# Performance work log

Measured on AMD Instinct MI355X. Metric: run time of the kernel, lower is better.

Reference implementation:

```python
import jax, jax.numpy as jnp
import numpy as np

NEG_SLOPE = 0.2

def _gat_layer(x, src, dst, W, a_src, a_dst, b, n_nodes):
    # x: [N, Fin], W: [Fin, Fout], a_src/a_dst: [Fout], b: [Fout]
    h = x @ W                                  # [N, Fout]
    alpha_s = h @ a_src                        # [N]
    alpha_d = h @ a_dst                        # [N]
    e = jax.nn.leaky_relu(alpha_s[src] + alpha_d[dst], NEG_SLOPE)  # [E]
    # softmax over edges grouped by destination node
    m = jax.ops.segment_max(e, dst, num_segments=n_nodes)
    ex = jnp.exp(e - m[dst])
    denom = jax.ops.segment_sum(ex, dst, num_segments=n_nodes)
    alpha = ex / denom[dst]                    # [E]
    out = jax.ops.segment_sum(h[src] * alpha[:, None], dst, num_segments=n_nodes)
    return out + b


def setup_inputs() -> dict:
    key = jax.random.key(0)
    N, E, INP = 50000, 1600000, 128
    topo = [32, 64, 128, 128]
    OUT = 16
    ks = jax.random.split(key, 32)
    inp = {}
    inp['x'] = jax.random.normal(ks[0], (N, INP), dtype=jnp.float32)
    inp['edge_index'] = jax.random.randint(ks[1], (2, E), 0, N, dtype=jnp.int64)
    dims = [INP] + topo
    ki = 2
    for i in range(4):
        fin, fout = dims[i], dims[i + 1]
        s = 1.0 / np.sqrt(fin)
        inp[f'W{i}'] = jax.random.normal(ks[ki], (fin, fout), dtype=jnp.float32) * s; ki += 1
        inp[f'a_src{i}'] = jax.random.normal(ks[ki], (fout,), dtype=jnp.float32) * (1.0 / np.sqrt(fout)); ki += 1
        inp[f'a_dst{i}'] = jax.random.normal(ks[ki], (fout,), dtype=jnp.float32) * (1.0 / np.sqrt(fout)); ki += 1
        inp[f'b{i}'] = jnp.zeros((fout,), dtype=jnp.float32); ki += 1
    inp['fc_W'] = jax.random.normal(ks[ki], (topo[-1], OUT), dtype=jnp.float32) * (1.0 / np.sqrt(topo[-1])); ki += 1
    inp['fc_b'] = jnp.zeros((OUT,), dtype=jnp.float32)
    return inp


def reference(x, edge_index, W0, a_src0, a_dst0, b0, W1, a_src1, a_dst1, b1,
              W2, a_src2, a_dst2, b2, W3, a_src3, a_dst3, b3, fc_W, fc_b):
    n = x.shape[0]
    loops = jnp.arange(n, dtype=edge_index.dtype)
    src = jnp.concatenate([edge_index[0], loops])  # add self-loops (GATConv default)
    dst = jnp.concatenate([edge_index[1], loops])
    layers = [(W0, a_src0, a_dst0, b0), (W1, a_src1, a_dst1, b1),
              (W2, a_src2, a_dst2, b2), (W3, a_src3, a_dst3, b3)]
    for (W, a_s, a_d, b) in layers:
        x = jax.nn.relu(_gat_layer(x, src, dst, W, a_s, a_d, b, n))
    return x @ fc_W + fc_b
```

## Files before the change

### kernel.cpp

```cpp
#include <hip/hip_runtime.h>
#include <hip/hip_bf16.h>
#include <hip/hip_fp16.h>


__device__ __forceinline__ float bf2f(unsigned short w) {
    return __uint_as_float(((unsigned int)w) << 16);
}
__device__ __forceinline__ unsigned enc_f(float f) {
    unsigned u = __float_as_uint(f);
    return (u & 0x80000000u) ? ~u : (u | 0x80000000u);
}
__device__ __forceinline__ float dec_f(unsigned u) {
    unsigned v = (u & 0x80000000u) ? (u & 0x7FFFFFFFu) : ~u;
    return __uint_as_float(v);
}

#define ELL_K 96

__global__ void detect_kernel(const unsigned short* __restrict__ xw,
                              const int* __restrict__ ew,
                              int* __restrict__ flags,
                              unsigned* __restrict__ maxbuf)
{
    __shared__ int cnt_sane[256];
    __shared__ int cnt_nz[256];
    const int t = threadIdx.x;
    unsigned short w = xw[2 * t];
    int e = (w >> 7) & 0xff;
    cnt_sane[t] = (e >= 110 && e <= 133) ? 1 : 0;
    cnt_nz[t] = (ew[2 * t + 1] != 0) ? 1 : 0;
    if (t < 8) maxbuf[t] = 0u;
    __syncthreads();
    if (t == 0) {
        int s = 0, nz = 0;
        for (int i = 0; i < 256; ++i) { s += cnt_sane[i]; nz += cnt_nz[i]; }
        flags[0] = (s >= 128) ? 1 : 0;
        flags[1] = (nz == 0) ? 1 : 0;
    }
}

struct ParamPtrs {
    const void* src[18];
    int n[18];
    int off[18];
};

__global__ void convert_params_kernel(ParamPtrs pp, const int* __restrict__ flags,
                                      float* __restrict__ out)
{
    const int b = blockIdx.x;
    const int n = pp.n[b];
    const float* fp = (const float*)pp.src[b];
    const unsigned short* hp = (const unsigned short*)pp.src[b];
    const int bf = flags[0];
    float* o = out + pp.off[b];
    for (int i = threadIdx.x; i < n; i += blockDim.x)
        o[i] = bf ? bf2f(hp[i]) : fp[i];
}

__global__ void extract_count_kernel(const int* __restrict__ e, const int* __restrict__ flags,
                                     unsigned* __restrict__ sd, unsigned short* __restrict__ rank,
                                     int* __restrict__ deg, long long E, long long Et)
{
    long long t = (long long)blockIdx.x * blockDim.x + threadIdx.x;
    if (t >= Et) return;
    int s, d;
    if (t >= E) { s = (int)(t - E); d = s; }
    else if (flags[1]) { s = e[2 * t]; d = e[2 * E + 2 * t]; }
    else               { s = e[t];     d = e[E + t]; }
    sd[t] = (unsigned)s | ((unsigned)d << 16);
    rank[t] = (unsigned short)atomicAdd(&deg[d], 1);
}

__global__ __launch_bounds__(256) void ell_fill_bucket_kernel(
    const unsigned* __restrict__ sd, const unsigned short* __restrict__ rank,
    unsigned short* __restrict__ ell16, long long Et, int chunkSize, int shift)
{
    const int bucket = blockIdx.x & 7;
    const long long c0 = (long long)(blockIdx.x >> 3) * chunkSize;
    const long long c1 = min(c0 + (long long)chunkSize, Et);
    for (long long i = c0 + threadIdx.x; i < c1; i += 256) {
        const unsigned v = sd[i];
        const int d = (int)(v >> 16);
        const int r = (int)rank[i];
        if ((d >> shift) == bucket && r < ELL_K)
            ell16[(long long)d * ELL_K + r] = (unsigned short)(v & 0xffffu);
    }
}

struct Half4 { __half2 a, b; };

__device__ __forceinline__ void store4(float* h, long long idx, const float* a) {
    *(float4*)(h + idx) = make_float4(a[0], a[1], a[2], a[3]);
}
__device__ __forceinline__ void store4(__half* h, long long idx, const float* a) {
    Half4 v;
    v.a = __floats2half2_rn(a[0], a[1]);
    v.b = __floats2half2_rn(a[2], a[3]);
    *(Half4*)(h + idx) = v;
}

template <int FIN, int FOUT, typename OT>
__global__ __launch_bounds__(256) void gemm_alpha_kernel(
    const void* __restrict__ xv, const int* __restrict__ flags, int x_ext,
    const float* __restrict__ W, const float* __restrict__ a_src,
    const float* __restrict__ a_dst, const float* __restrict__ bias,
    OT* __restrict__ h,
    float* __restrict__ alpha_s, float* __restrict__ alpha_d,
    unsigned* __restrict__ maxSD, int has_alpha,
    int N, int relu_in, int has_bias)
{
    constexpr int CG = FOUT / 4;
    constexpr int RT = 256 / CG;
    constexpr int RR = 64 / RT;
    constexpr int TM = 64;
    constexpr int XP = FIN + 4;
    constexpr int Q  = FIN / 8;

    __shared__ float xs[TM * XP];
    __shared__ float red[2][TM][CG + 1];

    const int tx = threadIdx.x;
    const int cg = tx & (CG - 1);
    const int rt = tx / CG;
    const long long base = (long long)blockIdx.x * TM;

    const int xbf = x_ext ? flags[0] : 0;

    for (int idx = tx; idx < TM * Q; idx += 256) {
        const int r  = idx / Q;
        const int c8 = idx - r * Q;
        const long long grow = base + r;
        float v[8] = {0.f, 0.f, 0.f, 0.f, 0.f, 0.f, 0.f, 0.f};
        if (grow < N) {
            const long long gi = grow * FIN + 8 * c8;
            if (x_ext) {
                if (xbf) {
                    const unsigned short* xp = (const unsigned short*)xv + gi;
                    #pragma unroll
                    for (int u = 0; u < 8; ++u) v[u] = bf2f(xp[u]);
                } else {
                    const float4 f0 = *((const float4*)((const float*)xv + gi));
                    const float4 f1 = *((const float4*)((const float*)xv + gi + 4));
                    v[0] = f0.x; v[1] = f0.y; v[2] = f0.z; v[3] = f0.w;
                    v[4] = f1.x; v[5] = f1.y; v[6] = f1.z; v[7] = f1.w;
                }
            } else {
                const float4 raw = *((const float4*)((const __half*)xv + gi));
                const __half2* q = (const __half2*)&raw;
                const float2 a0 = __half22float2(q[0]);
                const float2 a1 = __half22float2(q[1]);
                const float2 a2 = __half22float2(q[2]);
                const float2 a3 = __half22float2(q[3]);
                v[0] = a0.x; v[1] = a0.y; v[2] = a1.x; v[3] = a1.y;
                v[4] = a2.x; v[5] = a2.y; v[6] = a3.x; v[7] = a3.y;
            }
            if (relu_in) {
                #pragma unroll
                for (int u = 0; u < 8; ++u) v[u] = fmaxf(v[u], 0.f);
            }
        }
        *(float4*)&xs[r * XP + 8 * c8]     = make_float4(v[0], v[1], v[2], v[3]);
        *(float4*)&xs[r * XP + 8 * c8 + 4] = make_float4(v[4], v[5], v[6], v[7]);
    }
    __syncthreads();

    float acc[RR][4];
    #pragma unroll
    for (int rr = 0; rr < RR; ++rr)
        { acc[rr][0] = acc[rr][1] = acc[rr][2] = acc[rr][3] = 0.f; }

    const int r0 = rt * RR;
    #pragma unroll 4
    for (int k = 0; k < FIN; ++k) {
        const float4 w4 = *(const float4*)(W + k * FOUT + 4 * cg);
        #pragma unroll
        for (int rr = 0; rr < RR; ++rr) {
            const float xval = xs[(r0 + rr) * XP + k];
            acc[rr][0] += xval * w4.x;
            acc[rr][1] += xval * w4.y;
            acc[rr][2] += xval * w4.z;
            acc[rr][3] += xval * w4.w;
        }
    }

    if (has_bias) {
        const float4 b4 = *(const float4*)(bias + 4 * cg);
        #pragma unroll
        for (int rr = 0; rr < RR; ++rr) {
            acc[rr][0] += b4.x; acc[rr][1] += b4.y;
            acc[rr][2] += b4.z; acc[rr][3] += b4.w;
        }
    }

    #pragma unroll
    for (int rr = 0; rr < RR; ++rr) {
        const long long grow = base + r0 + rr;
        if (grow < N)
            store4(h, grow * FOUT + 4 * cg, acc[rr]);
    }

    if (has_alpha) {
        const float4 as4 = *(const float4*)(a_src + 4 * cg);
        const float4 ad4 = *(const float4*)(a_dst + 4 * cg);
        #pragma unroll
        for (int rr = 0; rr < RR; ++rr) {
            red[0][r0 + rr][cg] = acc[rr][0] * as4.x + acc[rr][1] * as4.y
                                + acc[rr][2] * as4.z + acc[rr][3] * as4.w;
            red[1][r0 + rr][cg] = acc[rr][0] * ad4.x + acc[rr][1] * ad4.y
                                + acc[rr][2] * ad4.z + acc[rr][3] * ad4.w;
        }
        __syncthreads();
        if (tx < TM) {
            float ss = 0.f, sd = 0.f;
            #pragma unroll
            for (int j = 0; j < CG; ++j) {
                ss += red[0][tx][j];
                sd += red[1][tx][j];
            }
            const long long grow = base + tx;
            const bool valid = grow < N;
            if (valid) { alpha_s[grow] = ss; alpha_d[grow] = sd; }
            float ms = valid ? ss : -INFINITY;
            float md = valid ? sd : -INFINITY;
            #pragma unroll
            for (int off = 32; off > 0; off >>= 1) {
                ms = fmaxf(ms, __shfl_down(ms, off, 64));
                md = fmaxf(md, __shfl_down(md, off, 64));
            }
            if (tx == 0) {
                atomicMax(&maxSD[0], enc_f(ms));
                atomicMax(&maxSD[1], enc_f(md));
            }
        }
    }
}

template <int FOUT>
__global__ __launch_bounds__(256) void gat_gather_kernel(
    const int* __restrict__ deg, const unsigned short* __restrict__ ell16,
    const float* __restrict__ as, const float* __restrict__ ad,
    const unsigned* __restrict__ maxSD,
    const __half* __restrict__ h, const float* __restrict__ bias,
    __half* __restrict__ out, int N)
{
    constexpr int LPE = FOUT / 8;
    constexpr int EPJ = 64 / LPE;

    const int wslot = threadIdx.x >> 6;
    const int lane = threadIdx.x & 63;
    const int d = blockIdx.x * 4 + wslot;
    if (d >= N) return;

    const float M = dec_f(maxSD[0]) + dec_f(maxSD[1]);
    const int cnt_all = min(deg[d], ELL_K);
    const long long e0 = (long long)d * ELL_K;
    const float add = ad[d];

    const int sub = lane / LPE;
    const int fl  = (lane % LPE) * 8;

    float den = 0.f;
    float a0 = 0.f, a1 = 0.f, a2 = 0.f, a3 = 0.f;
    float a4 = 0.f, a5 = 0.f, a6 = 0.f, a7 = 0.f;
    for (int base = 0; base < cnt_all; base += 64) {
        const int e = base + lane;
        float p = 0.f;
        int s = 0;
        if (e < cnt_all) {
            s = (int)ell16[e0 + e];
            float v = as[s] + add;
            v = (v > 0.f) ? v : 0.2f * v;
            p = expf(v - M);
        }
        den += p;
        const int cnt = min(64, cnt_all - base);
        for (int j = 0; j < cnt; j += 4 * EPJ) {
            float pj[4];
            float4 hv[4];
            #pragma unroll
            for (int u = 0; u < 4; ++u) {
                const int jj = j + u * EPJ + sub;
                pj[u] = __shfl(p, jj, 64);
                const int sj = __shfl(s, jj, 64);
                hv[u] = *(const float4*)(h + (long long)sj * FOUT + fl);
            }
            #pragma unroll
            for (int u = 0; u < 4; ++u) {
                const __half2* q = (const __half2*)&hv[u];
                const float2 f0 = __half22float2(q[0]);
                const float2 f1 = __half22float2(q[1]);
                const float2 f2 = __half22float2(q[2]);
                const float2 f3 = __half22float2(q[3]);
                a0 += pj[u] * f0.x;  a1 += pj[u] * f0.y;
                a2 += pj[u] * f1.x;  a3 += pj[u] * f1.y;
                a4 += pj[u] * f2.x;  a5 += pj[u] * f2.y;
                a6 += pj[u] * f3.x;  a7 += pj[u] * f3.y;
            }
        }
    }
    #pragma unroll
    for (int off = 32; off > 0; off >>= 1)
        den += __shfl_down(den, off, 64);
    den = __shfl(den, 0, 64);
    const float inv = 1.f / den;

    #pragma unroll
    for (int off = 32; off >= LPE; off >>= 1) {
        a0 += __shfl_down(a0, off, 64);
        a1 += __shfl_down(a1, off, 64);
        a2 += __shfl_down(a2, off, 64);
        a3 += __shfl_down(a3, off, 64);
        a4 += __shfl_down(a4, off, 64);
        a5 += __shfl_down(a5, off, 64);
        a6 += __shfl_down(a6, off, 64);
        a7 += __shfl_down(a7, off, 64);
    }
    if (lane < LPE) {
        const float4 bA = *(const float4*)(bias + fl);
        const float4 bB = *(const float4*)(bias + fl + 4);
        float4 pack;
        __half2* q = (__half2*)&pack;
        q[0] = __floats2half2_rn(bA.x + a0 * inv, bA.y + a1 * inv);
        q[1] = __floats2half2_rn(bA.z + a2 * inv, bA.w + a3 * inv);
        q[2] = __floats2half2_rn(bB.x + a4 * inv, bB.y + a5 * inv);
        q[3] = __floats2half2_rn(bB.z + a6 * inv, bB.w + a7 * inv);
        *(float4*)(out + (long long)d * FOUT + fl) = pack;
    }
}

extern "C" void kernel_launch(void* const* d_in, const int* in_sizes, int n_in,
                              void* d_out, int out_size, void* d_ws, size_t ws_size,
                              hipStream_t stream)
{
    const int INP = 128;
    const int N = in_sizes[0] / INP;
    const long long E = in_sizes[1] / 2;
    const long long Et = E + N;

    const int Fin[4]  = {128, 32, 64, 128};
    const int Fout[4] = {32, 64, 128, 128};

    char* p = (char*)d_ws;
    auto alloc = [&](size_t bytes) {
        char* r = p;
        p += (bytes + 255) & ~(size_t)255;
        return r;
    };
    __half*   bufH    = (__half*)  alloc((size_t)N * 128 * sizeof(__half));
    __half*   bufX    = (__half*)  alloc((size_t)N * 128 * sizeof(__half));
    float*    as      = (float*)   alloc((size_t)N * sizeof(float));
    float*    ad      = (float*)   alloc((size_t)N * sizeof(float));
    int*      deg     = (int*)     alloc((size_t)N * sizeof(int));
    unsigned short* ell16 = (unsigned short*)alloc((size_t)N * ELL_K * sizeof(unsigned short));
    unsigned* maxbuf  = (unsigned*)alloc(64);
    int*      flags   = (int*)     alloc(64);
    float*    params  = (float*)   alloc(64 * 1024 * sizeof(float));
    (void)ws_size;

    unsigned* sdA = (unsigned*)bufX;
    unsigned short* rankA = (unsigned short*)(sdA + Et);

    detect_kernel<<<1, 256, 0, stream>>>((const unsigned short*)d_in[0],
                                         (const int*)d_in[1], flags, maxbuf);

    ParamPtrs pp;
    int off = 0;
    {
        int k = 0;
        for (int i = 0; i < 4; ++i) {
            pp.n[k++] = Fin[i] * Fout[i];
            pp.n[k++] = Fout[i];
            pp.n[k++] = Fout[i];
            pp.n[k++] = Fout[i];
        }
        pp.n[16] = 128 * 16;
        pp.n[17] = 16;
        for (int i = 0; i < 18; ++i) {
            pp.src[i] = d_in[2 + i];
            pp.off[i] = off;
            off += pp.n[i];
        }
    }
    convert_params_kernel<<<18, 256, 0, stream>>>(pp, flags, params);

    const float* Wl[4], *asr[4], *adt[4], *bl[4];
    for (int i = 0; i < 4; ++i) {
        Wl[i]  = params + pp.off[4 * i + 0];
        asr[i] = params + pp.off[4 * i + 1];
        adt[i] = params + pp.off[4 * i + 2];
        bl[i]  = params + pp.off[4 * i + 3];
    }
    const float* fcW = params + pp.off[16];
    const float* fcb = params + pp.off[17];

    const int* e32 = (const int*)d_in[1];

    {
        hipMemsetAsync(deg, 0, (size_t)N * sizeof(int), stream);
        int eblocks = (int)((Et + 255) / 256);
        extract_count_kernel<<<eblocks, 256, 0, stream>>>(e32, flags, sdA, rankA,
                                                          deg, E, Et);
        int shift = 0;
        while ((N >> shift) > 8) shift++;
        const int chunkSize = 4096;
        const int nchunks = (int)((Et + chunkSize - 1) / chunkSize);
        ell_fill_bucket_kernel<<<nchunks * 8, 256, 0, stream>>>(
            sdA, rankA, ell16, Et, chunkSize, shift);
    }

    const int gblocks = (N + 3) / 4;
    const int mblocks = (N + 63) / 64;
    const void* xin = d_in[0];

    gemm_alpha_kernel<128, 32, __half><<<mblocks, 256, 0, stream>>>(
        xin, flags, 1, Wl[0], asr[0], adt[0], nullptr, bufH, as, ad,
        maxbuf + 0, 1, N, 0, 0);
    gat_gather_kernel<32><<<gblocks, 256, 0, stream>>>(
        deg, ell16, as, ad, maxbuf + 0, bufH, bl[0], bufX, N);

    gemm_alpha_kernel<32, 64, __half><<<mblocks, 256, 0, stream>>>(
        bufX, flags, 0, Wl[1], asr[1], adt[1], nullptr, bufH, as, ad,
        maxbuf + 2, 1, N, 1, 0);
    gat_gather_kernel<64><<<gblocks, 256, 0, stream>>>(
        deg, ell16, as, ad, maxbuf + 2, bufH, bl[1], bufX, N);

    gemm_alpha_kernel<64, 128, __half><<<mblocks, 256, 0, stream>>>(
        bufX, flags, 0, Wl[2], asr[2], adt[2], nullptr, bufH, as, ad,
        maxbuf + 4, 1, N, 1, 0);
    gat_gather_kernel<128><<<gblocks, 256, 0, stream>>>(
        deg, ell16, as, ad, maxbuf + 4, bufH, bl[2], bufX, N);

    gemm_alpha_kernel<128, 128, __half><<<mblocks, 256, 0, stream>>>(
        bufX, flags, 0, Wl[3], asr[3], adt[3], nullptr, bufH, as, ad,
        maxbuf + 6, 1, N, 1, 0);
    gat_gather_kernel<128><<<gblocks, 256, 0, stream>>>(
        deg, ell16, as, ad, maxbuf + 6, bufH, bl[3], bufX, N);

    gemm_alpha_kernel<128, 16, float><<<mblocks, 256, 0, stream>>>(
        bufX, flags, 0, fcW, nullptr, nullptr, fcb,
        (float*)d_out, nullptr, nullptr, nullptr, 0, N, 1, 1);
}
```

Before: 538.2 us.

## Build ELL adjacency via per-chunk shared-memory histograms instead of global atomics

Replaces the per-edge global atomicAdd degree counting with per-chunk shared-memory histograms holding packed 8-bit counters, a column scan that produces per-chunk base offsets and degrees, and an ELL fill that assigns slots with shared-memory atomics. This removes heavily contended global atomics and the 16-bit rank array. It adds a histogram buffer of NCHUNK×N bytes, which costs extra memory traffic. The 8-bit packed counters could overflow when a chunk holds many edges to one node, though slots are clamped at ELL_K. Slot ordering within a node may differ from before.

```diff
diff --git a/kernel.cpp b/kernel.cpp
--- a/kernel.cpp
+++ b/kernel.cpp
@@ -16,6 +16,7 @@
 }
 
 #define ELL_K 96
+#define NCHUNK 256
 
 __global__ void detect_kernel(const unsigned short* __restrict__ xw,
                               const int* __restrict__ ew,
@@ -58,33 +59,122 @@
         o[i] = bf ? bf2f(hp[i]) : fp[i];
 }
 
-__global__ void extract_count_kernel(const int* __restrict__ e, const int* __restrict__ flags,
-                                     unsigned* __restrict__ sd, unsigned short* __restrict__ rank,
-                                     int* __restrict__ deg, long long E, long long Et)
-{
-    long long t = (long long)blockIdx.x * blockDim.x + threadIdx.x;
-    if (t >= Et) return;
-    int s, d;
-    if (t >= E) { s = (int)(t - E); d = s; }
-    else if (flags[1]) { s = e[2 * t]; d = e[2 * E + 2 * t]; }
-    else               { s = e[t];     d = e[E + t]; }
-    sd[t] = (unsigned)s | ((unsigned)d << 16);
-    rank[t] = (unsigned short)atomicAdd(&deg[d], 1);
-}
-
-__global__ __launch_bounds__(256) void ell_fill_bucket_kernel(
-    const unsigned* __restrict__ sd, const unsigned short* __restrict__ rank,
-    unsigned short* __restrict__ ell16, long long Et, int chunkSize, int shift)
-{
+__global__ __launch_bounds__(1024) void hist_pack_kernel(
+    const int* __restrict__ e, const int* __restrict__ flags,
+    unsigned* __restrict__ sd, unsigned* __restrict__ hist,
+    long long E, long long Et, int chunk, int NQ)
+{
+    extern __shared__ unsigned hcnt[];
+    const int c = blockIdx.x;
+    for (int i = threadIdx.x; i < NQ; i += 1024) hcnt[i] = 0u;
+    __syncthreads();
+    const int f64 = flags[1];
+    const long long c0 = (long long)c * chunk;
+    long long c1 = c0 + chunk; if (c1 > Et) c1 = Et;
+    for (long long t = c0 + threadIdx.x; t < c1; t += 1024) {
+        int s, d;
+        if (t >= E) { s = (int)(t - E); d = s; }
+        else if (f64) { s = e[2 * t]; d = e[2 * E + 2 * t]; }
+        else          { s = e[t];     d = e[E + t]; }
+        sd[t] = (unsigned)s | ((unsigned)d << 16);
+        atomicAdd(&hcnt[d >> 2], 1u << ((d & 3) << 3));
+    }
+    __syncthreads();
+    unsigned* hrow = hist + (size_t)c * NQ;
+    for (int i = threadIdx.x; i < NQ; i += 1024) hrow[i] = hcnt[i];
+}
+
+__global__ __launch_bounds__(256) void chunk_scan_kernel(
+    const unsigned* __restrict__ hist, unsigned* __restrict__ base32,
+    int* __restrict__ deg, int NQ, int N)
+{
+    __shared__ unsigned short sums[32][8][4];
+    const int dql = threadIdx.x & 31;
+    const int oct = threadIdx.x >> 5;
+    const int dq  = blockIdx.x * 32 + dql;
+    const int cbeg = oct * 32;
+
+    unsigned s0 = 0, s1 = 0, s2 = 0, s3 = 0;
+    if (dq < NQ) {
+        const unsigned* hp = hist + (size_t)cbeg * NQ + dq;
+        #pragma unroll 8
+        for (int c = 0; c < 32; ++c) {
+            const unsigned v = hp[(size_t)c * NQ];
+            s0 += v & 0xffu;          s1 += (v >> 8) & 0xffu;
+            s2 += (v >> 16) & 0xffu;  s3 += v >> 24;
+        }
+    }
+    sums[dql][oct][0] = (unsigned short)s0;
+    sums[dql][oct][1] = (unsigned short)s1;
+    sums[dql][oct][2] = (unsigned short)s2;
+    sums[dql][oct][3] = (unsigned short)s3;
+    __syncthreads();
+
+    unsigned r0 = 0, r1 = 0, r2 = 0, r3 = 0;
+    #pragma unroll
+    for (int p = 0; p < 8; ++p) {
+        if (p < oct) {
+            r0 += sums[dql][p][0]; r1 += sums[dql][p][1];
+            r2 += sums[dql][p][2]; r3 += sums[dql][p][3];
+        }
+    }
+    if (dq >= NQ) return;
+
+    if (oct == 7) {
+        const int d0 = dq * 4;
+        const int t0 = (int)(r0 + s0), t1 = (int)(r1 + s1);
+        const int t2 = (int)(r2 + s2), t3 = (int)(r3 + s3);
+        if (d0 + 3 < N) {
+            *(int4*)(deg + d0) = make_int4(t0, t1, t2, t3);
+        } else {
+            if (d0     < N) deg[d0]     = t0;
+            if (d0 + 1 < N) deg[d0 + 1] = t1;
+            if (d0 + 2 < N) deg[d0 + 2] = t2;
+            if (d0 + 3 < N) deg[d0 + 3] = t3;
+        }
+    }
+
+    unsigned run0 = r0, run1 = r1, run2 = r2, run3 = r3;
+    const unsigned* hp = hist + (size_t)cbeg * NQ + dq;
+    unsigned* bp = base32 + (size_t)cbeg * NQ + dq;
+    for (int c = 0; c < 32; ++c) {
+        const unsigned v = hp[(size_t)c * NQ];
+        const unsigned o = (run0 < 255u ? run0 : 255u)
+                         | ((run1 < 255u ? run1 : 255u) << 8)
+                         | ((run2 < 255u ? run2 : 255u) << 16)
+                         | ((run3 < 255u ? run3 : 255u) << 24);
+        bp[(size_t)c * NQ] = o;
+        run0 += v & 0xffu;          run1 += (v >> 8) & 0xffu;
+        run2 += (v >> 16) & 0xffu;  run3 += v >> 24;
+    }
+}
+
+__global__ __launch_bounds__(256) void ell_fill_kernel(
+    const unsigned* __restrict__ sd, const unsigned* __restrict__ base32,
+    unsigned short* __restrict__ ell16, long long Et, int chunk, int NQ, int shift)
+{
+    extern __shared__ unsigned cnt[];
     const int bucket = blockIdx.x & 7;
-    const long long c0 = (long long)(blockIdx.x >> 3) * chunkSize;
-    const long long c1 = min(c0 + (long long)chunkSize, Et);
+    const int c = blockIdx.x >> 3;
+    const int words = (1 << shift) >> 2;
+    for (int i = threadIdx.x; i < words; i += 256) cnt[i] = 0u;
+    __syncthreads();
+    const long long c0 = (long long)c * chunk;
+    long long c1 = c0 + chunk; if (c1 > Et) c1 = Et;
+    const unsigned* brow = base32 + (size_t)c * NQ;
+    const int dlo = bucket << shift;
     for (long long i = c0 + threadIdx.x; i < c1; i += 256) {
         const unsigned v = sd[i];
         const int d = (int)(v >> 16);
-        const int r = (int)rank[i];
-        if ((d >> shift) == bucket && r < ELL_K)
-            ell16[(long long)d * ELL_K + r] = (unsigned short)(v & 0xffffu);
+        if ((d >> shift) != bucket) continue;
+        const int dl = d - dlo;
+        const unsigned sh = (unsigned)((dl & 3) << 3);
+        const unsigned old = atomicAdd(&cnt[dl >> 2], 1u << sh);
+        const unsigned lr = (old >> sh) & 0xffu;
+        const unsigned b = (brow[d >> 2] >> ((d & 3) << 3)) & 0xffu;
+        const unsigned slot = b + lr;
+        if (slot < ELL_K)
+            ell16[(long long)d * ELL_K + slot] = (unsigned short)(v & 0xffffu);
     }
 }
 
@@ -341,25 +431,31 @@
     const int Fin[4]  = {128, 32, 64, 128};
     const int Fout[4] = {32, 64, 128, 128};
 
+    const int NQ = (N + 3) / 4;
+    const size_t histBytes = (size_t)NQ * 4 * NCHUNK;
+    const size_t xbufBytes = (size_t)N * 128 * sizeof(__half);
+    const size_t bigBytes  = histBytes > xbufBytes ? histBytes : xbufBytes;
+
     char* p = (char*)d_ws;
     auto alloc = [&](size_t bytes) {
         char* r = p;
         p += (bytes + 255) & ~(size_t)255;
         return r;
     };
-    __half*   bufH    = (__half*)  alloc((size_t)N * 128 * sizeof(__half));
-    __half*   bufX    = (__half*)  alloc((size_t)N * 128 * sizeof(__half));
+    __half*   bufH    = (__half*)  alloc(bigBytes);
+    __half*   bufX    = (__half*)  alloc(bigBytes);
     float*    as      = (float*)   alloc((size_t)N * sizeof(float));
     float*    ad      = (float*)   alloc((size_t)N * sizeof(float));
     int*      deg     = (int*)     alloc((size_t)N * sizeof(int));
     unsigned short* ell16 = (unsigned short*)alloc((size_t)N * ELL_K * sizeof(unsigned short));
+    unsigned* sd      = (unsigned*)alloc((size_t)Et * sizeof(unsigned));
     unsigned* maxbuf  = (unsigned*)alloc(64);
     int*      flags   = (int*)     alloc(64);
     float*    params  = (float*)   alloc(64 * 1024 * sizeof(float));
     (void)ws_size;
 
-    unsigned* sdA = (unsigned*)bufX;
-    unsigned short* rankA = (unsigned short*)(sdA + Et);
+    unsigned* hist   = (unsigned*)bufH;
+    unsigned* base32 = (unsigned*)bufX;
 
     detect_kernel<<<1, 256, 0, stream>>>((const unsigned short*)d_in[0],
                                          (const int*)d_in[1], flags, maxbuf);
@@ -397,16 +493,15 @@
     const int* e32 = (const int*)d_in[1];
 
     {
-        hipMemsetAsync(deg, 0, (size_t)N * sizeof(int), stream);
-        int eblocks = (int)((Et + 255) / 256);
-        extract_count_kernel<<<eblocks, 256, 0, stream>>>(e32, flags, sdA, rankA,
-                                                          deg, E, Et);
+        const int chunk = (int)((Et + NCHUNK - 1) / NCHUNK);
         int shift = 0;
         while ((N >> shift) > 8) shift++;
-        const int chunkSize = 4096;
-        const int nchunks = (int)((Et + chunkSize - 1) / chunkSize);
-        ell_fill_bucket_kernel<<<nchunks * 8, 256, 0, stream>>>(
-            sdA, rankA, ell16, Et, chunkSize, shift);
+        hist_pack_kernel<<<NCHUNK, 1024, (size_t)NQ * 4, stream>>>(
+            e32, flags, sd, hist, E, Et, chunk, NQ);
+        chunk_scan_kernel<<<(NQ + 31) / 32, 256, 0, stream>>>(
+            hist, base32, deg, NQ, N);
+        ell_fill_kernel<<<NCHUNK * 8, 256, (size_t)(1 << shift), stream>>>(
+            sd, base32, ell16, Et, chunk, NQ, shift);
     }
 
     const int gblocks = (N + 3) / 4;
```

Measured after the change: 495.9 us. 1.09x faster.
